# Optimization experiments

Hardware: AMD Instinct MI355X
Metric: run time of the kernel (lower is better)

Reference implementation:

```python
import jax, jax.numpy as jnp
import numpy as np

BINS = 32
MAX_DIST = 128
EMB = 1024
DQ = 64
DV = 64
H = 16
B = 8
L = 1024


def _t5_bucket_table():
    # matches: clamp(n,max=m) + (log(clamp(n,min=m)-m+1)*(bins-1-m)/log(max_distance-m+1)).long()
    n = np.arange(MAX_DIST + 1)
    m = BINS // 2
    idx = np.minimum(n, m) + (
        np.log(np.maximum(n, m) - m + 1) * (BINS - 1 - m) / np.log(MAX_DIST - m + 1)
    ).astype(np.int64)
    return jnp.asarray(idx)


def setup_inputs() -> dict:
    key = jax.random.key(0)
    ks = jax.random.split(key, 8)
    s = 0.02
    return {
        "x": jax.random.normal(ks[0], (B, L, EMB), dtype=jnp.float32),
        "qk_w": jax.random.normal(ks[1], (2 * DQ * H, EMB), dtype=jnp.float32) * s,
        "qk_b": jnp.zeros((2 * DQ * H,), dtype=jnp.float32),
        "v_w": jax.random.normal(ks[2], (DV * H, EMB), dtype=jnp.float32) * s,
        "v_b": jnp.zeros((DV * H,), dtype=jnp.float32),
        "out_w": jax.random.normal(ks[3], (EMB, DV * H), dtype=jnp.float32) * s,
        "out_b": jnp.zeros((EMB,), dtype=jnp.float32),
        "bias": jax.random.normal(ks[4], (BINS, H), dtype=jnp.float32) * s,  # causal -> bins rows
    }


def reference(x, qk_w, qk_b, v_w, v_b, out_w, out_b, bias):
    # projections
    qk = (x @ qk_w.T + qk_b).reshape(B, L, H, 2 * DQ).transpose(0, 2, 1, 3)  # [B,H,L,2DQ]
    q, k = qk[..., :DQ], qk[..., DQ:]
    v = (x @ v_w.T + v_b).reshape(B, L, H, DV).transpose(0, 2, 1, 3)  # [B,H,L,DV]

    # T5 relative-position bias (causal): gather per (i-j) distance bucket
    idx_tab = _t5_bucket_table()
    shifts = jnp.arange(L)[:, None] - jnp.arange(L)[None, :]  # [L,L], i - j
    bins_idx = idx_tab[jnp.clip(jnp.abs(shifts), 0, MAX_DIST)]  # [L,L]
    bmat = bias[bins_idx].transpose(2, 0, 1)  # [H,L,L]
    bmat = jnp.where(shifts < 0, -jnp.inf, bmat)  # causal mask (j > i)

    scale = 1.0 / np.sqrt(DQ).astype(np.float32)
    scores = jnp.einsum("bhid,bhjd->bhij", q, k) * scale + bmat  # [B,H,L,L]
    attn = jax.nn.softmax(scores, axis=-1)
    out = jnp.einsum("bhij,bhjd->bhid", attn, v)  # [B,H,L,DV]
    out = out.transpose(0, 2, 1, 3).reshape(B, L, H * DV)
    return out @ out_w.T + out_b
```

## Files before the change

kernel.cpp:

```cpp
#include <hip/hip_runtime.h>
#include <cmath>


typedef _Float16 f16x8 __attribute__((ext_vector_type(8)));
typedef _Float16 f16x4 __attribute__((ext_vector_type(4)));
typedef float    f32x4 __attribute__((ext_vector_type(4)));

#define NEG_INF (-__builtin_inff())
#define LOG2E 1.4426950408889634f

#if __has_builtin(__builtin_amdgcn_exp2f)
#define EXP2(x) __builtin_amdgcn_exp2f(x)
#else
#define EXP2(x) exp2f(x)
#endif

__device__ __forceinline__ void gl_lds16(const void* g, void* l) {
  __builtin_amdgcn_global_load_lds(
      (__attribute__((address_space(1))) void*)g,
      (__attribute__((address_space(3))) void*)l,
      16, 0, 0);
}

__device__ __forceinline__ f32x4 mfma32(f16x8 a, f16x8 b, f32x4 c) {
  return __builtin_amdgcn_mfma_f32_16x16x32_f16(a, b, c, 0, 0, 0);
}
__device__ __forceinline__ f32x4 mfma16(f16x4 a, f16x4 b, f32x4 c) {
  return __builtin_amdgcn_mfma_f32_16x16x16f16(a, b, c, 0, 0, 0);
}

__global__ void cvt_kernel(const float* __restrict__ in,
                           _Float16* __restrict__ out, int n4) {
  int i = blockIdx.x * blockDim.x + threadIdx.x;
  if (i >= n4) return;
  float4 v = reinterpret_cast<const float4*>(in)[i];
  f16x4 o;
  o[0] = (_Float16)v.x; o[1] = (_Float16)v.y;
  o[2] = (_Float16)v.z; o[3] = (_Float16)v.w;
  reinterpret_cast<f16x4*>(out)[i] = o;
}

template <int MODE>
__global__ __launch_bounds__(256, 2) void gemm_kernel(
    const _Float16* __restrict__ A, const _Float16* __restrict__ Bm,
    int M, int N, int K,
    const float* __restrict__ bias_q, const float* __restrict__ bias_v,
    _Float16* __restrict__ qkbuf, _Float16* __restrict__ vtbuf,
    const float* __restrict__ bias_o, float* __restrict__ outf) {
  __shared__ __align__(16) _Float16 lds_a[128 * 32];
  __shared__ __align__(16) _Float16 lds_b[128 * 32];
  const int t = threadIdx.x;
  const int w = t >> 6;
  const int lane = t & 63;
  const int lq = lane & 15, lg = lane >> 4;
  const int wr = w >> 1, wc = w & 1;
  const int m0 = blockIdx.y * 128, n0 = blockIdx.x * 128;

  const _Float16* pA0 = A + (size_t)(m0 + (t >> 2)) * K + (t & 3) * 8;
  const _Float16* pA1 = pA0 + (size_t)64 * K;
  const _Float16* pB0 = Bm + (size_t)(n0 + (t >> 2)) * K + (t & 3) * 8;
  const _Float16* pB1 = pB0 + (size_t)64 * K;
  _Float16* la0 = &lds_a[(w * 64) * 8];
  _Float16* la1 = &lds_a[(256 + w * 64) * 8];
  _Float16* lb0 = &lds_b[(w * 64) * 8];
  _Float16* lb1 = &lds_b[(256 + w * 64) * 8];

  f32x4 acc[4][4];
#pragma unroll
  for (int mi = 0; mi < 4; ++mi)
#pragma unroll
    for (int ni = 0; ni < 4; ++ni) acc[mi][ni] = (f32x4){0.f, 0.f, 0.f, 0.f};

  for (int k0 = 0; k0 < K; k0 += 32) {
    __syncthreads();
    gl_lds16(pA0 + k0, la0);
    gl_lds16(pA1 + k0, la1);
    gl_lds16(pB0 + k0, lb0);
    gl_lds16(pB1 + k0, lb1);
    __syncthreads();
    f16x8 af[4], bfr[4];
#pragma unroll
    for (int mi = 0; mi < 4; ++mi)
      af[mi] = *(const f16x8*)&lds_a[(wr * 64 + mi * 16 + lq) * 32 + lg * 8];
#pragma unroll
    for (int ni = 0; ni < 4; ++ni)
      bfr[ni] = *(const f16x8*)&lds_b[(wc * 64 + ni * 16 + lq) * 32 + lg * 8];
#pragma unroll
    for (int mi = 0; mi < 4; ++mi)
#pragma unroll
      for (int ni = 0; ni < 4; ++ni)
        acc[mi][ni] = mfma32(af[mi], bfr[ni], acc[mi][ni]);
  }

  if (MODE == 0) {
    const bool isqk = (n0 < 2048);
#pragma unroll
    for (int mi = 0; mi < 4; ++mi)
#pragma unroll
      for (int ni = 0; ni < 4; ++ni)
#pragma unroll
        for (int r = 0; r < 4; ++r) {
          const int mg = m0 + wr * 64 + mi * 16 + lg * 4 + r;
          const int ng = n0 + wc * 64 + ni * 16 + lq;
          const int bb = mg >> 10, ii = mg & 1023;
          float val = acc[mi][ni][r];
          if (isqk) {
            val += bias_q[ng];
            const int hh = ng >> 7, cc = ng & 127;
            qkbuf[((size_t)((bb * 16 + hh) * 1024 + ii)) * 128 + cc] =
                (_Float16)val;
          } else {
            const int nn = ng - 2048;
            val += bias_v[nn];
            const int hh = nn >> 6, dv = nn & 63;
            vtbuf[((size_t)((bb * 16 + hh) * 64 + dv)) * 1024 + ii] =
                (_Float16)val;
          }
        }
  } else {
#pragma unroll
    for (int mi = 0; mi < 4; ++mi)
#pragma unroll
      for (int ni = 0; ni < 4; ++ni)
#pragma unroll
        for (int r = 0; r < 4; ++r) {
          const int mg = m0 + wr * 64 + mi * 16 + lg * 4 + r;
          const int ng = n0 + wc * 64 + ni * 16 + lq;
          outf[(size_t)mg * N + ng] = acc[mi][ni][r] + bias_o[ng];
        }
  }
}

__device__ __forceinline__ void stage_kv(const _Float16* __restrict__ kb,
                                         const _Float16* __restrict__ vtb,
                                         int j0, _Float16* kl, _Float16* vl,
                                         int t) {
  const int r0 = t >> 3, c0 = t & 7;
  const int r1 = r0 + 32;
  const int kc0 = c0 ^ (r0 & 7), kc1 = c0 ^ (r1 & 7);
  gl_lds16(kb + (size_t)(j0 + r0) * 128 + kc0 * 8, kl + t * 8);
  gl_lds16(kb + (size_t)(j0 + r1) * 128 + kc1 * 8, kl + (t + 256) * 8);
  gl_lds16(vtb + (size_t)r0 * 1024 + j0 + kc0 * 8, vl + t * 8);
  gl_lds16(vtb + (size_t)r1 * 1024 + j0 + kc1 * 8, vl + (t + 256) * 8);
}

__device__ __forceinline__ void softmax16(f32x4 (&st)[4], f16x4 (&ph)[4],
                                          int qi, int j0, bool far,
                                          const float* __restrict__ tab,
                                          float t128, int lg4, float& m_run,
                                          float& l_part, f32x4 (&oacc)[4]) {
  float xs[16];
  float lmax = NEG_INF;
  if (far) {
#pragma unroll
    for (int js = 0; js < 4; ++js)
#pragma unroll
      for (int r = 0; r < 4; ++r) {
        const float xv = fmaf(st[js][r], 0.125f * LOG2E, t128);
        xs[js * 4 + r] = xv;
        lmax = fmaxf(lmax, xv);
      }
  } else {
#pragma unroll
    for (int js = 0; js < 4; ++js)
#pragma unroll
      for (int r = 0; r < 4; ++r) {
        const int jj = j0 + js * 16 + lg4 + r;
        const int dd = qi - jj;
        const int idx = dd < 0 ? 0 : (dd > 128 ? 128 : dd);
        const float xv =
            (dd < 0) ? NEG_INF : fmaf(st[js][r], 0.125f * LOG2E, tab[idx]);
        xs[js * 4 + r] = xv;
        lmax = fmaxf(lmax, xv);
      }
  }
  if (__any(lmax > m_run + 8.0f)) {
    float tmax = fmaxf(lmax, __shfl_xor(lmax, 16));
    tmax = fmaxf(tmax, __shfl_xor(tmax, 32));
    const float m_new = fmaxf(m_run, tmax);
    const float sf = EXP2(m_run - m_new);
    m_run = m_new;
    l_part *= sf;
    f32x4 sfv;
#pragma unroll
    for (int r = 0; r < 4; ++r) sfv[r] = __shfl(sf, lg4 + r);
#pragma unroll
    for (int db = 0; db < 4; ++db) oacc[db] *= sfv;
  }
  float ls = 0.f;
#pragma unroll
  for (int js = 0; js < 4; ++js)
#pragma unroll
    for (int r = 0; r < 4; ++r) {
      const float p = EXP2(xs[js * 4 + r] - m_run);
      ls += p;
      ph[js][r] = (_Float16)p;
    }
  l_part += ls;
}

__global__ __launch_bounds__(256, 4) void attn_kernel(
    const _Float16* __restrict__ qk,
    const _Float16* __restrict__ vt,
    const float* __restrict__ bias,
    _Float16* __restrict__ ao) {
  __shared__ __align__(16) _Float16 kls[2][64 * 64];
  __shared__ __align__(16) _Float16 vls[2][64 * 64];
  __shared__ float tab[132];
  const int t = threadIdx.x;
  const int bid = blockIdx.x;
  const int bh = (bid & 7) * 16 + (bid >> 6);
  const int b4 = (bid >> 3) & 7;
  const int h = bh & 15, b = bh >> 4;
  if (t < 129) {
    const int bucket =
        (t <= 16) ? t : 16 + (int)(log((double)(t - 15)) * 15.0 / log(113.0));
    tab[t] = bias[bucket * 16 + h] * LOG2E;
  }

  const int w = t >> 6, lane = t & 63;
  const int lq = lane & 15, lg = lane >> 4;
  const int lg4 = lg * 4, lg8 = lg * 8;
  const int tA = b4, tB = 15 - b4;
  const int q0A = tA * 64 + w * 16, q0B = tB * 64 + w * 16;
  const int qA = q0A + lq, qB = q0B + lq;
  const _Float16* qkb = qk + (size_t)bh * 1024 * 128;
  const _Float16* kb = qkb + 64;
  const _Float16* vtb = vt + (size_t)bh * 64 * 1024;

  const f16x8 qfA0 = *(const f16x8*)&qkb[qA * 128 + lg8];
  const f16x8 qfA1 = *(const f16x8*)&qkb[qA * 128 + 32 + lg8];
  const f16x8 qfB0 = *(const f16x8*)&qkb[qB * 128 + lg8];
  const f16x8 qfB1 = *(const f16x8*)&qkb[qB * 128 + 32 + lg8];

  f32x4 oA[4], oB[4];
#pragma unroll
  for (int db = 0; db < 4; ++db) {
    oA[db] = (f32x4){0.f, 0.f, 0.f, 0.f};
    oB[db] = (f32x4){0.f, 0.f, 0.f, 0.f};
  }
  float mA = NEG_INF, lAp = 0.f, mB = NEG_INF, lBp = 0.f;

  stage_kv(kb, vtb, 0, kls[0], vls[0], t);
  __syncthreads();
  const float t128 = tab[128];
  const int krsw = lq & 7;
  const int vsw = (lq & 7) << 1;
  int cur = 0;

  for (int jt = 0; jt <= tB; ++jt) {
    const int j0 = jt * 64;
    if (jt < tB) stage_kv(kb, vtb, j0 + 64, kls[cur ^ 1], vls[cur ^ 1], t);
    const bool aact = (jt <= tA);
    const _Float16* kbf = kls[cur];
    const _Float16* vbf = vls[cur];

    f32x4 stA[4], stB[4];
#pragma unroll
    for (int js = 0; js < 4; ++js) {
      const int rowb = (js * 16 + lq) * 64;
      const f16x8 kf0 = *(const f16x8*)&kbf[rowb + ((lg ^ krsw) << 3)];
      const f16x8 kf1 = *(const f16x8*)&kbf[rowb + (((lg + 4) ^ krsw) << 3)];
      if (aact) {
        stA[js] = mfma32(kf0, qfA0, (f32x4){0.f, 0.f, 0.f, 0.f});
        stA[js] = mfma32(kf1, qfA1, stA[js]);
      }
      stB[js] = mfma32(kf0, qfB0, (f32x4){0.f, 0.f, 0.f, 0.f});
      stB[js] = mfma32(kf1, qfB1, stB[js]);
    }

    f16x4 phA[4], phB[4];
    if (aact)
      softmax16(stA, phA, qA, j0, q0A - j0 >= 192, tab, t128, lg4, mA, lAp,
                oA);
    softmax16(stB, phB, qB, j0, q0B - j0 >= 192, tab, t128, lg4, mB, lBp, oB);

#pragma unroll
    for (int js = 0; js < 4; ++js)
#pragma unroll
      for (int db = 0; db < 4; ++db) {
        const f16x4 vf = *(const f16x4*)&vbf[(db * 16 + lq) * 64 +
                                             ((((js << 2) + lg) ^ vsw) << 2)];
        if (aact) oA[db] = mfma16(phA[js], vf, oA[db]);
        oB[db] = mfma16(phB[js], vf, oB[db]);
      }

    __syncthreads();
    cur ^= 1;
  }

  _Float16* aob = ao + ((size_t)b * 1024) * 1024 + h * 64;
  {
    float lt = lAp + __shfl_xor(lAp, 16);
    lt += __shfl_xor(lt, 32);
    f32x4 linv;
#pragma unroll
    for (int r = 0; r < 4; ++r) linv[r] = 1.0f / __shfl(lt, lg4 + r);
#pragma unroll
    for (int db = 0; db < 4; ++db)
#pragma unroll
      for (int r = 0; r < 4; ++r)
        aob[(size_t)(q0A + lg4 + r) * 1024 + db * 16 + lq] =
            (_Float16)(oA[db][r] * linv[r]);
  }
  {
    float lt = lBp + __shfl_xor(lBp, 16);
    lt += __shfl_xor(lt, 32);
    f32x4 linv;
#pragma unroll
    for (int r = 0; r < 4; ++r) linv[r] = 1.0f / __shfl(lt, lg4 + r);
#pragma unroll
    for (int db = 0; db < 4; ++db)
#pragma unroll
      for (int r = 0; r < 4; ++r)
        aob[(size_t)(q0B + lg4 + r) * 1024 + db * 16 + lq] =
            (_Float16)(oB[db][r] * linv[r]);
  }
}

extern "C" void kernel_launch(void* const* d_in, const int* in_sizes, int n_in,
                              void* d_out, int out_size, void* d_ws,
                              size_t ws_size, hipStream_t stream) {
  const float* x = (const float*)d_in[0];
  const float* qk_w = (const float*)d_in[1];
  const float* qk_b = (const float*)d_in[2];
  const float* v_w = (const float*)d_in[3];
  const float* v_b = (const float*)d_in[4];
  const float* out_w = (const float*)d_in[5];
  const float* out_b = (const float*)d_in[6];
  const float* bias = (const float*)d_in[7];
  float* out = (float*)d_out;

  _Float16* xb = (_Float16*)d_ws;
  _Float16* wb = xb + (size_t)8388608;
  _Float16* owb = wb + (size_t)3145728;
  _Float16* qkbuf = owb + (size_t)1048576;
  _Float16* vtbuf = qkbuf + (size_t)16777216;
  _Float16* ao = vtbuf + (size_t)8388608;

  cvt_kernel<<<8192, 256, 0, stream>>>(x, xb, 2097152);
  cvt_kernel<<<2048, 256, 0, stream>>>(qk_w, wb, 524288);
  cvt_kernel<<<1024, 256, 0, stream>>>(v_w, wb + 2097152, 262144);
  cvt_kernel<<<1024, 256, 0, stream>>>(out_w, owb, 262144);

  gemm_kernel<0><<<dim3(24, 64), 256, 0, stream>>>(
      xb, wb, 8192, 3072, 1024, qk_b, v_b, qkbuf, vtbuf, nullptr, nullptr);

  attn_kernel<<<1024, 256, 0, stream>>>(qkbuf, vtbuf, bias, ao);

  gemm_kernel<1><<<dim3(8, 64), 256, 0, stream>>>(
      ao, owb, 8192, 1024, 1024, nullptr, nullptr, nullptr, nullptr, out_b, out);
}
```

Measured before the change: 193.5 us.

## Double-buffer GEMM LDS tiles and prefetch next K-slice during MFMA

Switches the projection GEMM kernel from single-buffered LDS to ping-pong buffers. The next K-slice is loaded via global_load_lds while MFMAs run on the current slice, leaving one barrier per iteration instead of two. It also raises wave priority around the MFMA block. The aim is to hide global load latency, at the cost of doubling LDS per block (32KB), which could affect occupancy at 2 blocks per CU.

```diff
diff --git a/kernel.cpp b/kernel.cpp
--- a/kernel.cpp
+++ b/kernel.cpp
@@ -47,8 +47,8 @@
     const float* __restrict__ bias_q, const float* __restrict__ bias_v,
     _Float16* __restrict__ qkbuf, _Float16* __restrict__ vtbuf,
     const float* __restrict__ bias_o, float* __restrict__ outf) {
-  __shared__ __align__(16) _Float16 lds_a[128 * 32];
-  __shared__ __align__(16) _Float16 lds_b[128 * 32];
+  __shared__ __align__(16) _Float16 lds_a[2][128 * 32];
+  __shared__ __align__(16) _Float16 lds_b[2][128 * 32];
   const int t = threadIdx.x;
   const int w = t >> 6;
   const int lane = t & 63;
@@ -60,10 +60,7 @@
   const _Float16* pA1 = pA0 + (size_t)64 * K;
   const _Float16* pB0 = Bm + (size_t)(n0 + (t >> 2)) * K + (t & 3) * 8;
   const _Float16* pB1 = pB0 + (size_t)64 * K;
-  _Float16* la0 = &lds_a[(w * 64) * 8];
-  _Float16* la1 = &lds_a[(256 + w * 64) * 8];
-  _Float16* lb0 = &lds_b[(w * 64) * 8];
-  _Float16* lb1 = &lds_b[(256 + w * 64) * 8];
+  const int wofs = w * 512;
 
   f32x4 acc[4][4];
 #pragma unroll
@@ -71,25 +68,39 @@
 #pragma unroll
     for (int ni = 0; ni < 4; ++ni) acc[mi][ni] = (f32x4){0.f, 0.f, 0.f, 0.f};
 
+  gl_lds16(pA0, &lds_a[0][wofs]);
+  gl_lds16(pA1, &lds_a[0][2048 + wofs]);
+  gl_lds16(pB0, &lds_b[0][wofs]);
+  gl_lds16(pB1, &lds_b[0][2048 + wofs]);
+  __syncthreads();
+
+  int cur = 0;
   for (int k0 = 0; k0 < K; k0 += 32) {
-    __syncthreads();
-    gl_lds16(pA0 + k0, la0);
-    gl_lds16(pA1 + k0, la1);
-    gl_lds16(pB0 + k0, lb0);
-    gl_lds16(pB1 + k0, lb1);
-    __syncthreads();
+    const int nx = cur ^ 1;
+    if (k0 + 32 < K) {
+      gl_lds16(pA0 + k0 + 32, &lds_a[nx][wofs]);
+      gl_lds16(pA1 + k0 + 32, &lds_a[nx][2048 + wofs]);
+      gl_lds16(pB0 + k0 + 32, &lds_b[nx][wofs]);
+      gl_lds16(pB1 + k0 + 32, &lds_b[nx][2048 + wofs]);
+    }
     f16x8 af[4], bfr[4];
 #pragma unroll
     for (int mi = 0; mi < 4; ++mi)
-      af[mi] = *(const f16x8*)&lds_a[(wr * 64 + mi * 16 + lq) * 32 + lg * 8];
+      af[mi] =
+          *(const f16x8*)&lds_a[cur][(wr * 64 + mi * 16 + lq) * 32 + lg * 8];
 #pragma unroll
     for (int ni = 0; ni < 4; ++ni)
-      bfr[ni] = *(const f16x8*)&lds_b[(wc * 64 + ni * 16 + lq) * 32 + lg * 8];
+      bfr[ni] =
+          *(const f16x8*)&lds_b[cur][(wc * 64 + ni * 16 + lq) * 32 + lg * 8];
+    __builtin_amdgcn_s_setprio(1);
 #pragma unroll
     for (int mi = 0; mi < 4; ++mi)
 #pragma unroll
       for (int ni = 0; ni < 4; ++ni)
         acc[mi][ni] = mfma32(af[mi], bfr[ni], acc[mi][ni]);
+    __builtin_amdgcn_s_setprio(0);
+    __syncthreads();
+    cur = nx;
   }
 
   if (MODE == 0) {
```

New measurement: 194.6 us. No clear change (+0.5%).

## Pipeline GEMM mainloop with 4-stage LDS ring, swizzle and interleaved MFMA

Applied to the files above, without the earlier changes.

Replaces the synchronous load-then-compute GEMM loop with a 4-buffer LDS ring, so global-to-LDS loads for later k-steps are issued while MFMAs run on the current one. It adds an XOR swizzle on the LDS layout to reduce bank conflicts, and uses hand-written ds_read with explicit waitcnt, setprio and a single barrier per step. The loop is hardcoded for K=1024 (32 k-steps), so other K values would be wrong. LDS use grows fourfold to 64KB per block, which may limit occupancy at 2 blocks per CU.

```diff
diff --git a/kernel.cpp b/kernel.cpp
--- a/kernel.cpp
+++ b/kernel.cpp
@@ -28,6 +28,8 @@
 __device__ __forceinline__ f32x4 mfma16(f16x4 a, f16x4 b, f32x4 c) {
   return __builtin_amdgcn_mfma_f32_16x16x16f16(a, b, c, 0, 0, 0);
 }
+
+typedef __attribute__((address_space(3))) _Float16* lds_f16p;
 
 __global__ void cvt_kernel(const float* __restrict__ in,
                            _Float16* __restrict__ out, int n4) {
@@ -40,6 +42,66 @@
   reinterpret_cast<f16x4*>(out)[i] = o;
 }
 
+#define LGKM0                                          \
+  asm volatile("s_waitcnt lgkmcnt(0)" ::: "memory");   \
+  __builtin_amdgcn_sched_barrier(0)
+#define DSR(d, a, o) \
+  asm volatile("ds_read_b128 %0, %1 offset:" o : "=v"(d) : "v"(a))
+
+#define GEMM_STAGE(buf, kk)                         \
+  do {                                              \
+    gl_lds16(pA0 + (kk), &lds_a[buf][wofs]);        \
+    gl_lds16(pA1 + (kk), &lds_a[buf][2048 + wofs]); \
+    gl_lds16(pB0 + (kk), &lds_b[buf][wofs]);        \
+    gl_lds16(pB1 + (kk), &lds_b[buf][2048 + wofs]); \
+  } while (0)
+
+#define GEMM_STEP(aB, bB, sb, kk, VMC)                            \
+  do {                                                            \
+    asm volatile("s_waitcnt vmcnt(" VMC ")" ::: "memory");        \
+    __builtin_amdgcn_s_barrier();                                 \
+    f16x8 af0, af1, af2, af3, bf0, bf1, bf2, bf3;                 \
+    DSR(af0, aB, "0");                                            \
+    DSR(bf0, bB, "0");                                            \
+    DSR(af1, aB, "1024");                                         \
+    DSR(bf1, bB, "1024");                                         \
+    if ((sb) >= 0) gl_lds16(pA0 + (kk), &lds_a[(sb)][wofs]);      \
+    LGKM0;                                                        \
+    __builtin_amdgcn_s_setprio(1);                                \
+    acc[0][0] = mfma32(af0, bf0, acc[0][0]);                      \
+    acc[0][1] = mfma32(af0, bf1, acc[0][1]);                      \
+    acc[1][0] = mfma32(af1, bf0, acc[1][0]);                      \
+    acc[1][1] = mfma32(af1, bf1, acc[1][1]);                      \
+    __builtin_amdgcn_s_setprio(0);                                \
+    DSR(af2, aB, "2048");                                         \
+    DSR(af3, aB, "3072");                                         \
+    if ((sb) >= 0) gl_lds16(pA1 + (kk), &lds_a[(sb)][2048 + wofs]); \
+    LGKM0;                                                        \
+    __builtin_amdgcn_s_setprio(1);                                \
+    acc[2][0] = mfma32(af2, bf0, acc[2][0]);                      \
+    acc[2][1] = mfma32(af2, bf1, acc[2][1]);                      \
+    acc[3][0] = mfma32(af3, bf0, acc[3][0]);                      \
+    acc[3][1] = mfma32(af3, bf1, acc[3][1]);                      \
+    __builtin_amdgcn_s_setprio(0);                                \
+    DSR(bf2, bB, "2048");                                         \
+    DSR(bf3, bB, "3072");                                         \
+    if ((sb) >= 0) gl_lds16(pB0 + (kk), &lds_b[(sb)][wofs]);      \
+    LGKM0;                                                        \
+    __builtin_amdgcn_s_setprio(1);                                \
+    acc[0][2] = mfma32(af0, bf2, acc[0][2]);                      \
+    acc[0][3] = mfma32(af0, bf3, acc[0][3]);                      \
+    acc[1][2] = mfma32(af1, bf2, acc[1][2]);                      \
+    acc[1][3] = mfma32(af1, bf3, acc[1][3]);                      \
+    __builtin_amdgcn_s_setprio(0);                                \
+    if ((sb) >= 0) gl_lds16(pB1 + (kk), &lds_b[(sb)][2048 + wofs]); \
+    __builtin_amdgcn_s_setprio(1);                                \
+    acc[2][2] = mfma32(af2, bf2, acc[2][2]);                      \
+    acc[2][3] = mfma32(af2, bf3, acc[2][3]);                      \
+    acc[3][2] = mfma32(af3, bf2, acc[3][2]);                      \
+    acc[3][3] = mfma32(af3, bf3, acc[3][3]);                      \
+    __builtin_amdgcn_s_setprio(0);                                \
+  } while (0)
+
 template <int MODE>
 __global__ __launch_bounds__(256, 2) void gemm_kernel(
     const _Float16* __restrict__ A, const _Float16* __restrict__ Bm,
@@ -47,8 +109,8 @@
     const float* __restrict__ bias_q, const float* __restrict__ bias_v,
     _Float16* __restrict__ qkbuf, _Float16* __restrict__ vtbuf,
     const float* __restrict__ bias_o, float* __restrict__ outf) {
-  __shared__ __align__(16) _Float16 lds_a[128 * 32];
-  __shared__ __align__(16) _Float16 lds_b[128 * 32];
+  __shared__ __align__(16) _Float16 lds_a[4][128 * 32];
+  __shared__ __align__(16) _Float16 lds_b[4][128 * 32];
   const int t = threadIdx.x;
   const int w = t >> 6;
   const int lane = t & 63;
@@ -56,14 +118,22 @@
   const int wr = w >> 1, wc = w & 1;
   const int m0 = blockIdx.y * 128, n0 = blockIdx.x * 128;
 
-  const _Float16* pA0 = A + (size_t)(m0 + (t >> 2)) * K + (t & 3) * 8;
+  const int stc = ((t & 3) ^ ((t >> 3) & 3)) * 8;
+  const _Float16* pA0 = A + (size_t)(m0 + (t >> 2)) * K + stc;
   const _Float16* pA1 = pA0 + (size_t)64 * K;
-  const _Float16* pB0 = Bm + (size_t)(n0 + (t >> 2)) * K + (t & 3) * 8;
+  const _Float16* pB0 = Bm + (size_t)(n0 + (t >> 2)) * K + stc;
   const _Float16* pB1 = pB0 + (size_t)64 * K;
-  _Float16* la0 = &lds_a[(w * 64) * 8];
-  _Float16* la1 = &lds_a[(256 + w * 64) * 8];
-  _Float16* lb0 = &lds_b[(w * 64) * 8];
-  _Float16* lb1 = &lds_b[(256 + w * 64) * 8];
+  const int wofs = w * 512;
+
+  const int xsw = (lq >> 1) & 3;
+  const uint32_t aBv = (uint32_t)(uintptr_t)(lds_f16p)&lds_a[0][0] +
+                       (uint32_t)((wr * 64 + lq) * 64 + ((lg ^ xsw) << 4));
+  const uint32_t bBv = (uint32_t)(uintptr_t)(lds_f16p)&lds_b[0][0] +
+                       (uint32_t)((wc * 64 + lq) * 64 + ((lg ^ xsw) << 4));
+  const uint32_t aB0 = aBv, aB1 = aBv + 8192, aB2 = aBv + 16384,
+                 aB3 = aBv + 24576;
+  const uint32_t bB0 = bBv, bB1 = bBv + 8192, bB2 = bBv + 16384,
+                 bB3 = bBv + 24576;
 
   f32x4 acc[4][4];
 #pragma unroll
@@ -71,26 +141,20 @@
 #pragma unroll
     for (int ni = 0; ni < 4; ++ni) acc[mi][ni] = (f32x4){0.f, 0.f, 0.f, 0.f};
 
-  for (int k0 = 0; k0 < K; k0 += 32) {
-    __syncthreads();
-    gl_lds16(pA0 + k0, la0);
-    gl_lds16(pA1 + k0, la1);
-    gl_lds16(pB0 + k0, lb0);
-    gl_lds16(pB1 + k0, lb1);
-    __syncthreads();
-    f16x8 af[4], bfr[4];
-#pragma unroll
-    for (int mi = 0; mi < 4; ++mi)
-      af[mi] = *(const f16x8*)&lds_a[(wr * 64 + mi * 16 + lq) * 32 + lg * 8];
-#pragma unroll
-    for (int ni = 0; ni < 4; ++ni)
-      bfr[ni] = *(const f16x8*)&lds_b[(wc * 64 + ni * 16 + lq) * 32 + lg * 8];
-#pragma unroll
-    for (int mi = 0; mi < 4; ++mi)
-#pragma unroll
-      for (int ni = 0; ni < 4; ++ni)
-        acc[mi][ni] = mfma32(af[mi], bfr[ni], acc[mi][ni]);
-  }
+  GEMM_STAGE(0, 0);
+  GEMM_STAGE(1, 32);
+  GEMM_STAGE(2, 64);
+  for (int s = 0; s < 28; s += 4) {
+    const int kk = (s + 3) * 32;
+    GEMM_STEP(aB0, bB0, 3, kk, "8");
+    GEMM_STEP(aB1, bB1, 0, kk + 32, "8");
+    GEMM_STEP(aB2, bB2, 1, kk + 64, "8");
+    GEMM_STEP(aB3, bB3, 2, kk + 96, "8");
+  }
+  GEMM_STEP(aB0, bB0, 3, 992, "8");
+  GEMM_STEP(aB1, bB1, -1, 0, "8");
+  GEMM_STEP(aB2, bB2, -1, 0, "4");
+  GEMM_STEP(aB3, bB3, -1, 0, "0");
 
   if (MODE == 0) {
     const bool isqk = (n0 < 2048);
```

Result: no change. 192.6 us (-0.5%).
